# Performance work log

Hardware: AMD Instinct MI355X
Metric: run time of the kernel (lower is better)

## Reference

```python
import jax, jax.numpy as jnp
import numpy as np

N_NODES = 100000
N_EDGES = 1600000
NFEAT, NHID, NCLASS = 64, 128, 32


def _glorot(key, shape):
    fan_in, fan_out = shape[0], shape[1]
    lim = np.sqrt(6.0 / (fan_in + fan_out))
    return jax.random.uniform(key, shape, jnp.float32, -lim, lim)


def setup_inputs() -> dict:
    key = jax.random.key(0)
    ks = jax.random.split(key, 12)
    x = jax.random.normal(ks[0], (N_NODES, NFEAT), jnp.float32)
    edge_idx = jax.random.randint(ks[1], (2, N_EDGES), 0, N_NODES, jnp.int64)
    edge_weight = jax.random.uniform(ks[2], (N_EDGES,), jnp.float32)
    return {
        "x": x,
        "edge_idx": edge_idx,
        "edge_weight": edge_weight,
        # SAGEConv 1: out = mean_agg(x) @ Wl1 + b1 + x @ Wr1
        "Wl1": _glorot(ks[3], (NFEAT, NHID)),
        "Wr1": _glorot(ks[4], (NFEAT, NHID)),
        "b1": jnp.zeros((NHID,), jnp.float32),
        # SAGEConv 2
        "Wl2": _glorot(ks[5], (NHID, NHID)),
        "Wr2": _glorot(ks[6], (NHID, NHID)),
        "b2": jnp.zeros((NHID,), jnp.float32),
        # fc head: Linear(nhid, nclass) -> Linear(nclass, 1)
        "Wfc1": _glorot(ks[7], (NHID, NCLASS)),
        "bfc1": jnp.zeros((NCLASS,), jnp.float32),
        "Wfc2": _glorot(ks[8], (NCLASS, 1)),
        "bfc2": jnp.zeros((1,), jnp.float32),
    }


def _sage_conv(x, src, dst, Wl, Wr, b, n_nodes):
    # mean aggregation of source features at destination nodes
    msg_sum = jax.ops.segment_sum(x[src], dst, num_segments=n_nodes)  # [N, d]
    deg = jax.ops.segment_sum(jnp.ones((src.shape[0], 1), x.dtype), dst,
                              num_segments=n_nodes)                    # [N, 1]
    mean = msg_sum / jnp.maximum(deg, 1.0)
    return mean @ Wl + b + x @ Wr


def reference(x, edge_idx, edge_weight, Wl1, Wr1, b1, Wl2, Wr2, b2,
              Wfc1, bfc1, Wfc2, bfc2):
    n_nodes = x.shape[0]
    src, dst = edge_idx[0], edge_idx[1]
    # dropout is identity in eval mode (training=False)
    h = _sage_conv(x, src, dst, Wl1, Wr1, b1, n_nodes)   # [N, nhid]
    h = _sage_conv(h, src, dst, Wl2, Wr2, b2, n_nodes)   # [N, nhid]
    h = h @ Wfc1 + bfc1                                   # [N, nclass]
    out = h @ Wfc2 + bfc2                                 # [N, 1]
    return out
```

## Files before the change

### kernel.cpp

```cpp
#include <hip/hip_runtime.h>

#define S_SHIFT 9
#define S_NODES 512
#define CAP     10240
#define CHUNK   4096
#define NREP    4
#define DGRID   256

__global__ __launch_bounds__(1024) void fold_dots_kernel(
    const float* __restrict__ x,
    const float* __restrict__ Wl1, const float* __restrict__ Wr1, const float* __restrict__ b1,
    const float* __restrict__ Wl2, const float* __restrict__ Wr2, const float* __restrict__ b2,
    const float* __restrict__ Wfc1, const float* __restrict__ bfc1,
    const float* __restrict__ Wfc2, const float* __restrict__ bfc2,
    float* __restrict__ ga, float2* __restrict__ gbc, float* __restrict__ c01,
    int* __restrict__ cursor, int N)
{
    __shared__ float wv[192];
    __shared__ float uu[128], vl2[128], vr2[128], w2[32];
    int t = threadIdx.x;
    int l = t & 63;
    int w = t >> 6;

    if (blockIdx.x == 0 && t < 256) cursor[t] = 0;
    if (t < 32) w2[t] = Wfc2[t];
    __syncthreads();
    for (int j = 0; j < 8; ++j) {
        int i = w + 16 * j;
        float p = (l < 32) ? Wfc1[i * 32 + l] * w2[l] : 0.f;
        for (int m = 16; m; m >>= 1) p += __shfl_xor(p, m);
        if (l == 0) uu[i] = p;
    }
    __syncthreads();
    for (int j = 0; j < 8; ++j) {
        int i = w + 16 * j;
        float ua = uu[l], ub = uu[64 + l];
        float pa = Wl2[i * 128 + l] * ua + Wl2[i * 128 + 64 + l] * ub;
        float pb = Wr2[i * 128 + l] * ua + Wr2[i * 128 + 64 + l] * ub;
        for (int m = 32; m; m >>= 1) { pa += __shfl_xor(pa, m); pb += __shfl_xor(pb, m); }
        if (l == 0) { vl2[i] = pa; vr2[i] = pb; }
    }
    __syncthreads();
    for (int j = 0; j < 4; ++j) {
        int i = w + 16 * j;
        float l1a = Wl1[i * 128 + l], l1b = Wl1[i * 128 + 64 + l];
        float r1a = Wr1[i * 128 + l], r1b = Wr1[i * 128 + 64 + l];
        float La = vl2[l], Lb = vl2[64 + l], Ra = vr2[l], Rb = vr2[64 + l];
        float pc = l1a * La + l1b * Lb;
        float pb = l1a * Ra + l1b * Rb + r1a * La + r1b * Lb;
        float pa = r1a * Ra + r1b * Rb;
        for (int m = 32; m; m >>= 1) {
            pa += __shfl_xor(pa, m); pb += __shfl_xor(pb, m); pc += __shfl_xor(pc, m);
        }
        if (l == 0) { wv[i] = pa; wv[64 + i] = pb; wv[128 + i] = pc; }
    }
    if (blockIdx.x == 0 && w == 15) {
        float p0 = b1[l] * vr2[l] + b1[64 + l] * vr2[64 + l]
                 + b2[l] * uu[l] + b2[64 + l] * uu[64 + l];
        if (l < 32) p0 += bfc1[l] * w2[l];
        float p1 = b1[l] * vl2[l] + b1[64 + l] * vl2[64 + l];
        for (int m = 32; m; m >>= 1) { p0 += __shfl_xor(p0, m); p1 += __shfl_xor(p1, m); }
        if (l == 0) { c01[0] = p0 + bfc2[0]; c01[1] = p1; }
    }
    __syncthreads();

    int fp = l & 15, sub = l >> 4;
    float4 wa4 = ((const float4*)wv)[fp];
    float4 wb4 = ((const float4*)wv)[16 + fp];
    float4 wc4 = ((const float4*)wv)[32 + fp];
    const float4* x4 = (const float4*)x;
    int Q = (N + 3) >> 2;
    for (int qd = blockIdx.x * 16 + w; qd < Q; qd += DGRID * 16) {
        int node = qd * 4 + sub;
        float a = 0.f, b = 0.f, c = 0.f;
        if (node < N) {
            float4 v = x4[(size_t)node * 16 + fp];
            a = v.x * wa4.x + v.y * wa4.y + v.z * wa4.z + v.w * wa4.w;
            b = v.x * wb4.x + v.y * wb4.y + v.z * wb4.z + v.w * wb4.w;
            c = v.x * wc4.x + v.y * wc4.y + v.z * wc4.z + v.w * wc4.w;
        }
        for (int m = 8; m; m >>= 1) {
            a += __shfl_xor(a, m); b += __shfl_xor(b, m); c += __shfl_xor(c, m);
        }
        if (fp == 0 && node < N) { ga[node] = a; gbc[node] = make_float2(b, c); }
    }
}

__global__ __launch_bounds__(256) void scatter_kernel(
    const int* __restrict__ src, const int* __restrict__ dst, int E, int B,
    int* __restrict__ cursor, unsigned* __restrict__ bucket)
{
    __shared__ int hist[256], lbase[256], lcur[256];
    int t = threadIdx.x;
    int e0 = blockIdx.x * CHUNK;
    int cnt = E - e0; if (cnt > CHUNK) cnt = CHUNK;
    hist[t] = 0;
    __syncthreads();
    for (int i = t; i < cnt; i += 256)
        atomicAdd(&hist[dst[e0 + i] >> S_SHIFT], 1);
    __syncthreads();
    if (t < B && hist[t] > 0) lbase[t] = atomicAdd(&cursor[t], hist[t]);
    lcur[t] = 0;
    __syncthreads();
    for (int i = t; i < cnt; i += 256) {
        int d = dst[e0 + i], s = src[e0 + i];
        int b = d >> S_SHIFT;
        int off = atomicAdd(&lcur[b], 1);
        bucket[(size_t)b * CAP + (unsigned)(lbase[b] + off)] =
            ((unsigned)s << S_SHIFT) | (unsigned)(d & (S_NODES - 1));
    }
}

__global__ __launch_bounds__(1024) void aggA_kernel(
    const unsigned* __restrict__ bucket, const int* __restrict__ cursor,
    const float2* __restrict__ gbc, const float* __restrict__ ga,
    const float* __restrict__ c01,
    float* __restrict__ q, float* __restrict__ t1, float* __restrict__ inv, int N)
{
    __shared__ float aB[NREP][S_NODES], aC[NREP][S_NODES];
    __shared__ int cnt[NREP][S_NODES];
    int t = threadIdx.x, b = blockIdx.x;
    int r = (t >> 6) & (NREP - 1);
    float* aBf = (float*)aB; float* aCf = (float*)aC; int* cnf = (int*)cnt;
    for (int i = t; i < NREP * S_NODES; i += 1024) { aBf[i] = 0.f; aCf[i] = 0.f; cnf[i] = 0; }
    __syncthreads();
    int n = cursor[b];
    const unsigned* bp = bucket + (size_t)b * CAP;
    for (int i = t; i < n; i += 1024) {
        unsigned uu = bp[i];
        float2 g = gbc[uu >> S_SHIFT];
        int dl = uu & (S_NODES - 1);
        atomicAdd(&aB[r][dl], g.x);
        atomicAdd(&aC[r][dl], g.y);
        atomicAdd(&cnt[r][dl], 1);
    }
    __syncthreads();
    if (t < S_NODES) {
        int node = (b << S_SHIFT) + t;
        if (node < N) {
            float sb = aB[0][t] + aB[1][t] + aB[2][t] + aB[3][t];
            float sc = aC[0][t] + aC[1][t] + aC[2][t] + aC[3][t];
            int d = cnt[0][t] + cnt[1][t] + cnt[2][t] + cnt[3][t];
            float iv = 1.0f / ((d > 0) ? (float)d : 1.0f);
            inv[node] = iv;
            q[node]   = iv * sc;
            t1[node]  = ga[node] + iv * sb + c01[0] + (d > 0 ? c01[1] : 0.f);
        }
    }
}

__global__ __launch_bounds__(1024) void aggB_kernel(
    const unsigned* __restrict__ bucket, const int* __restrict__ cursor,
    const float* __restrict__ q, const float* __restrict__ t1,
    const float* __restrict__ inv, float* __restrict__ out, int N)
{
    __shared__ float a2[NREP][S_NODES];
    int t = threadIdx.x, b = blockIdx.x;
    int r = (t >> 6) & (NREP - 1);
    float* a2f = (float*)a2;
    for (int i = t; i < NREP * S_NODES; i += 1024) a2f[i] = 0.f;
    __syncthreads();
    int n = cursor[b];
    const unsigned* bp = bucket + (size_t)b * CAP;
    for (int i = t; i < n; i += 1024) {
        unsigned uu = bp[i];
        atomicAdd(&a2[r][uu & (S_NODES - 1)], q[uu >> S_SHIFT]);
    }
    __syncthreads();
    if (t < S_NODES) {
        int node = (b << S_SHIFT) + t;
        if (node < N)
            out[node] = t1[node] + inv[node] * (a2[0][t] + a2[1][t] + a2[2][t] + a2[3][t]);
    }
}

extern "C" void kernel_launch(void* const* d_in, const int* in_sizes, int n_in,
                              void* d_out, int out_size, void* d_ws, size_t ws_size,
                              hipStream_t stream) {
    const float* x    = (const float*)d_in[0];
    const int*   eidx = (const int*)d_in[1];
    const float* Wl1  = (const float*)d_in[3];
    const float* Wr1  = (const float*)d_in[4];
    const float* b1   = (const float*)d_in[5];
    const float* Wl2  = (const float*)d_in[6];
    const float* Wr2  = (const float*)d_in[7];
    const float* b2   = (const float*)d_in[8];
    const float* Wfc1 = (const float*)d_in[9];
    const float* bfc1 = (const float*)d_in[10];
    const float* Wfc2 = (const float*)d_in[11];
    const float* bfc2 = (const float*)d_in[12];

    const int N = in_sizes[0] / 64;
    const int E = in_sizes[2];
    const int* src = eidx;
    const int* dst = eidx + E;
    const int B = (N + S_NODES - 1) / S_NODES;
    const int nscat = (E + CHUNK - 1) / CHUNK;

    char* ws = (char*)d_ws;
    int*      cursor = (int*)(ws);
    float*    c01    = (float*)(ws + 1024);
    float*    ga     = (float*)(ws + 2048);
    float*    q      = (float*)(ws + 2048 + (size_t)N * 4);
    float*    t1     = (float*)(ws + 2048 + (size_t)N * 8);
    float*    inv    = (float*)(ws + 2048 + (size_t)N * 12);
    float2*   gbc    = (float2*)(ws + 2048 + (size_t)N * 16);
    unsigned* bucket = (unsigned*)(ws + 2048 + (size_t)N * 24);

    fold_dots_kernel<<<DGRID, 1024, 0, stream>>>(
        x, Wl1, Wr1, b1, Wl2, Wr2, b2, Wfc1, bfc1, Wfc2, bfc2,
        ga, gbc, c01, cursor, N);

    scatter_kernel<<<nscat, 256, 0, stream>>>(src, dst, E, B, cursor, bucket);

    aggA_kernel<<<B, 1024, 0, stream>>>(bucket, cursor, gbc, ga, c01, q, t1, inv, N);
    aggB_kernel<<<B, 1024, 0, stream>>>(bucket, cursor, q, t1, inv, (float*)d_out, N);
}
```

Before: 174.5 us.

## Fuse edge scatter and node dot-products into one kernel with smaller buckets

Merges the weight-folding/dot-product kernel and the edge bucketing scatter into one launch, with disjoint block ranges doing each job, so the two independent phases overlap and one launch is saved. The cursor reset becomes a memset because the fused kernel cannot zero it before the scatter blocks use it. Buckets shrink from 512 to 256 nodes (400 buckets, smaller capacity) and the aggregation kernels move to 512 threads, giving more blocks for load balance. The cost is an extra memset launch and a higher risk of bucket overflow with the smaller capacity under skewed degree distributions.

```diff
diff --git a/kernel.cpp b/kernel.cpp
--- a/kernel.cpp
+++ b/kernel.cpp
@@ -1,117 +1,117 @@
 #include <hip/hip_runtime.h>
 
-#define S_SHIFT 9
-#define S_NODES 512
-#define CAP     10240
-#define CHUNK   4096
+#define S_SHIFT 8
+#define S_NODES 256
+#define NBKT    400
+#define CAP     5120
+#define CHUNK   8192
 #define NREP    4
-#define DGRID   256
-
-__global__ __launch_bounds__(1024) void fold_dots_kernel(
+#define FTH     512
+#define NDOTS   160
+
+__global__ __launch_bounds__(FTH) void fused_kernel(
     const float* __restrict__ x,
+    const int* __restrict__ src, const int* __restrict__ dst,
+    int E, int N, int B, int nscat,
+    int* __restrict__ cursor, unsigned* __restrict__ bucket,
     const float* __restrict__ Wl1, const float* __restrict__ Wr1, const float* __restrict__ b1,
     const float* __restrict__ Wl2, const float* __restrict__ Wr2, const float* __restrict__ b2,
     const float* __restrict__ Wfc1, const float* __restrict__ bfc1,
     const float* __restrict__ Wfc2, const float* __restrict__ bfc2,
-    float* __restrict__ ga, float2* __restrict__ gbc, float* __restrict__ c01,
-    int* __restrict__ cursor, int N)
+    float* __restrict__ ga, float2* __restrict__ gbc, float* __restrict__ c01)
 {
-    __shared__ float wv[192];
-    __shared__ float uu[128], vl2[128], vr2[128], w2[32];
+    __shared__ int hist[NBKT], lbase[NBKT], lcur[NBKT];
+    __shared__ float wv[192], uu[128], vl2[128], vr2[128], w2[32];
     int t = threadIdx.x;
     int l = t & 63;
     int w = t >> 6;
 
-    if (blockIdx.x == 0 && t < 256) cursor[t] = 0;
-    if (t < 32) w2[t] = Wfc2[t];
-    __syncthreads();
-    for (int j = 0; j < 8; ++j) {
-        int i = w + 16 * j;
-        float p = (l < 32) ? Wfc1[i * 32 + l] * w2[l] : 0.f;
-        for (int m = 16; m; m >>= 1) p += __shfl_xor(p, m);
-        if (l == 0) uu[i] = p;
-    }
-    __syncthreads();
-    for (int j = 0; j < 8; ++j) {
-        int i = w + 16 * j;
-        float ua = uu[l], ub = uu[64 + l];
-        float pa = Wl2[i * 128 + l] * ua + Wl2[i * 128 + 64 + l] * ub;
-        float pb = Wr2[i * 128 + l] * ua + Wr2[i * 128 + 64 + l] * ub;
-        for (int m = 32; m; m >>= 1) { pa += __shfl_xor(pa, m); pb += __shfl_xor(pb, m); }
-        if (l == 0) { vl2[i] = pa; vr2[i] = pb; }
-    }
-    __syncthreads();
-    for (int j = 0; j < 4; ++j) {
-        int i = w + 16 * j;
-        float l1a = Wl1[i * 128 + l], l1b = Wl1[i * 128 + 64 + l];
-        float r1a = Wr1[i * 128 + l], r1b = Wr1[i * 128 + 64 + l];
-        float La = vl2[l], Lb = vl2[64 + l], Ra = vr2[l], Rb = vr2[64 + l];
-        float pc = l1a * La + l1b * Lb;
-        float pb = l1a * Ra + l1b * Rb + r1a * La + r1b * Lb;
-        float pa = r1a * Ra + r1b * Rb;
-        for (int m = 32; m; m >>= 1) {
-            pa += __shfl_xor(pa, m); pb += __shfl_xor(pb, m); pc += __shfl_xor(pc, m);
-        }
-        if (l == 0) { wv[i] = pa; wv[64 + i] = pb; wv[128 + i] = pc; }
-    }
-    if (blockIdx.x == 0 && w == 15) {
-        float p0 = b1[l] * vr2[l] + b1[64 + l] * vr2[64 + l]
-                 + b2[l] * uu[l] + b2[64 + l] * uu[64 + l];
-        if (l < 32) p0 += bfc1[l] * w2[l];
-        float p1 = b1[l] * vl2[l] + b1[64 + l] * vl2[64 + l];
-        for (int m = 32; m; m >>= 1) { p0 += __shfl_xor(p0, m); p1 += __shfl_xor(p1, m); }
-        if (l == 0) { c01[0] = p0 + bfc2[0]; c01[1] = p1; }
-    }
-    __syncthreads();
-
-    int fp = l & 15, sub = l >> 4;
-    float4 wa4 = ((const float4*)wv)[fp];
-    float4 wb4 = ((const float4*)wv)[16 + fp];
-    float4 wc4 = ((const float4*)wv)[32 + fp];
-    const float4* x4 = (const float4*)x;
-    int Q = (N + 3) >> 2;
-    for (int qd = blockIdx.x * 16 + w; qd < Q; qd += DGRID * 16) {
-        int node = qd * 4 + sub;
-        float a = 0.f, b = 0.f, c = 0.f;
-        if (node < N) {
-            float4 v = x4[(size_t)node * 16 + fp];
-            a = v.x * wa4.x + v.y * wa4.y + v.z * wa4.z + v.w * wa4.w;
-            b = v.x * wb4.x + v.y * wb4.y + v.z * wb4.z + v.w * wb4.w;
-            c = v.x * wc4.x + v.y * wc4.y + v.z * wc4.z + v.w * wc4.w;
-        }
-        for (int m = 8; m; m >>= 1) {
-            a += __shfl_xor(a, m); b += __shfl_xor(b, m); c += __shfl_xor(c, m);
-        }
-        if (fp == 0 && node < N) { ga[node] = a; gbc[node] = make_float2(b, c); }
-    }
-}
-
-__global__ __launch_bounds__(256) void scatter_kernel(
-    const int* __restrict__ src, const int* __restrict__ dst, int E, int B,
-    int* __restrict__ cursor, unsigned* __restrict__ bucket)
-{
-    __shared__ int hist[256], lbase[256], lcur[256];
-    int t = threadIdx.x;
-    int e0 = blockIdx.x * CHUNK;
-    int cnt = E - e0; if (cnt > CHUNK) cnt = CHUNK;
-    hist[t] = 0;
-    __syncthreads();
-    for (int i = t; i < cnt; i += 256)
-        atomicAdd(&hist[dst[e0 + i] >> S_SHIFT], 1);
-    __syncthreads();
-    if (t < B && hist[t] > 0) lbase[t] = atomicAdd(&cursor[t], hist[t]);
-    lcur[t] = 0;
-    __syncthreads();
-    for (int i = t; i < cnt; i += 256) {
-        int d = dst[e0 + i], s = src[e0 + i];
-        int b = d >> S_SHIFT;
-        int off = atomicAdd(&lcur[b], 1);
-        bucket[(size_t)b * CAP + (unsigned)(lbase[b] + off)] =
-            ((unsigned)s << S_SHIFT) | (unsigned)(d & (S_NODES - 1));
-    }
-}
-
-__global__ __launch_bounds__(1024) void aggA_kernel(
+    if ((int)blockIdx.x < nscat) {
+        int e0 = blockIdx.x * CHUNK;
+        int cnt = E - e0; if (cnt > CHUNK) cnt = CHUNK;
+        for (int i = t; i < B; i += FTH) hist[i] = 0;
+        __syncthreads();
+        for (int i = t; i < cnt; i += FTH)
+            atomicAdd(&hist[dst[e0 + i] >> S_SHIFT], 1);
+        __syncthreads();
+        for (int i = t; i < B; i += FTH) {
+            lcur[i] = 0;
+            if (hist[i] > 0) lbase[i] = atomicAdd(&cursor[i], hist[i]);
+        }
+        __syncthreads();
+        for (int i = t; i < cnt; i += FTH) {
+            int d = dst[e0 + i], s = src[e0 + i];
+            int bb = d >> S_SHIFT;
+            int off = atomicAdd(&lcur[bb], 1);
+            bucket[(size_t)bb * CAP + (unsigned)(lbase[bb] + off)] =
+                ((unsigned)s << S_SHIFT) | (unsigned)(d & (S_NODES - 1));
+        }
+    } else {
+        if (t < 32) w2[t] = Wfc2[t];
+        __syncthreads();
+        for (int j = 0; j < 16; ++j) {
+            int i = w + 8 * j;
+            float p = (l < 32) ? Wfc1[i * 32 + l] * w2[l] : 0.f;
+            for (int m = 16; m; m >>= 1) p += __shfl_xor(p, m);
+            if (l == 0) uu[i] = p;
+        }
+        __syncthreads();
+        for (int j = 0; j < 16; ++j) {
+            int i = w + 8 * j;
+            float ua = uu[l], ub = uu[64 + l];
+            float pa = Wl2[i * 128 + l] * ua + Wl2[i * 128 + 64 + l] * ub;
+            float pb = Wr2[i * 128 + l] * ua + Wr2[i * 128 + 64 + l] * ub;
+            for (int m = 32; m; m >>= 1) { pa += __shfl_xor(pa, m); pb += __shfl_xor(pb, m); }
+            if (l == 0) { vl2[i] = pa; vr2[i] = pb; }
+        }
+        __syncthreads();
+        for (int j = 0; j < 8; ++j) {
+            int i = w + 8 * j;
+            float l1a = Wl1[i * 128 + l], l1b = Wl1[i * 128 + 64 + l];
+            float r1a = Wr1[i * 128 + l], r1b = Wr1[i * 128 + 64 + l];
+            float La = vl2[l], Lb = vl2[64 + l], Ra = vr2[l], Rb = vr2[64 + l];
+            float pc = l1a * La + l1b * Lb;
+            float pb = l1a * Ra + l1b * Rb + r1a * La + r1b * Lb;
+            float pa = r1a * Ra + r1b * Rb;
+            for (int m = 32; m; m >>= 1) {
+                pa += __shfl_xor(pa, m); pb += __shfl_xor(pb, m); pc += __shfl_xor(pc, m);
+            }
+            if (l == 0) { wv[i] = pa; wv[64 + i] = pb; wv[128 + i] = pc; }
+        }
+        if ((int)blockIdx.x == nscat && w == 7) {
+            float p0 = b1[l] * vr2[l] + b1[64 + l] * vr2[64 + l]
+                     + b2[l] * uu[l] + b2[64 + l] * uu[64 + l];
+            if (l < 32) p0 += bfc1[l] * w2[l];
+            float p1 = b1[l] * vl2[l] + b1[64 + l] * vl2[64 + l];
+            for (int m = 32; m; m >>= 1) { p0 += __shfl_xor(p0, m); p1 += __shfl_xor(p1, m); }
+            if (l == 0) { c01[0] = p0 + bfc2[0]; c01[1] = p1; }
+        }
+        __syncthreads();
+
+        int fp = l & 15, sub = l >> 4;
+        float4 wa4 = ((const float4*)wv)[fp];
+        float4 wb4 = ((const float4*)wv)[16 + fp];
+        float4 wc4 = ((const float4*)wv)[32 + fp];
+        const float4* x4 = (const float4*)x;
+        int Q = (N + 3) >> 2;
+        for (int qd = ((int)blockIdx.x - nscat) * 8 + w; qd < Q; qd += NDOTS * 8) {
+            int node = qd * 4 + sub;
+            float a = 0.f, b = 0.f, c = 0.f;
+            if (node < N) {
+                float4 v = x4[(size_t)node * 16 + fp];
+                a = v.x * wa4.x + v.y * wa4.y + v.z * wa4.z + v.w * wa4.w;
+                b = v.x * wb4.x + v.y * wb4.y + v.z * wb4.z + v.w * wb4.w;
+                c = v.x * wc4.x + v.y * wc4.y + v.z * wc4.z + v.w * wc4.w;
+            }
+            for (int m = 8; m; m >>= 1) {
+                a += __shfl_xor(a, m); b += __shfl_xor(b, m); c += __shfl_xor(c, m);
+            }
+            if (fp == 0 && node < N) { ga[node] = a; gbc[node] = make_float2(b, c); }
+        }
+    }
+}
+
+__global__ __launch_bounds__(512) void aggA_kernel(
     const unsigned* __restrict__ bucket, const int* __restrict__ cursor,
     const float2* __restrict__ gbc, const float* __restrict__ ga,
     const float* __restrict__ c01,
@@ -122,11 +122,11 @@
     int t = threadIdx.x, b = blockIdx.x;
     int r = (t >> 6) & (NREP - 1);
     float* aBf = (float*)aB; float* aCf = (float*)aC; int* cnf = (int*)cnt;
-    for (int i = t; i < NREP * S_NODES; i += 1024) { aBf[i] = 0.f; aCf[i] = 0.f; cnf[i] = 0; }
+    for (int i = t; i < NREP * S_NODES; i += 512) { aBf[i] = 0.f; aCf[i] = 0.f; cnf[i] = 0; }
     __syncthreads();
     int n = cursor[b];
     const unsigned* bp = bucket + (size_t)b * CAP;
-    for (int i = t; i < n; i += 1024) {
+    for (int i = t; i < n; i += 512) {
         unsigned uu = bp[i];
         float2 g = gbc[uu >> S_SHIFT];
         int dl = uu & (S_NODES - 1);
@@ -149,7 +149,7 @@
     }
 }
 
-__global__ __launch_bounds__(1024) void aggB_kernel(
+__global__ __launch_bounds__(512) void aggB_kernel(
     const unsigned* __restrict__ bucket, const int* __restrict__ cursor,
     const float* __restrict__ q, const float* __restrict__ t1,
     const float* __restrict__ inv, float* __restrict__ out, int N)
@@ -158,11 +158,11 @@
     int t = threadIdx.x, b = blockIdx.x;
     int r = (t >> 6) & (NREP - 1);
     float* a2f = (float*)a2;
-    for (int i = t; i < NREP * S_NODES; i += 1024) a2f[i] = 0.f;
+    for (int i = t; i < NREP * S_NODES; i += 512) a2f[i] = 0.f;
     __syncthreads();
     int n = cursor[b];
     const unsigned* bp = bucket + (size_t)b * CAP;
-    for (int i = t; i < n; i += 1024) {
+    for (int i = t; i < n; i += 512) {
         unsigned uu = bp[i];
         atomicAdd(&a2[r][uu & (S_NODES - 1)], q[uu >> S_SHIFT]);
     }
@@ -199,20 +199,21 @@
 
     char* ws = (char*)d_ws;
     int*      cursor = (int*)(ws);
-    float*    c01    = (float*)(ws + 1024);
-    float*    ga     = (float*)(ws + 2048);
-    float*    q      = (float*)(ws + 2048 + (size_t)N * 4);
-    float*    t1     = (float*)(ws + 2048 + (size_t)N * 8);
-    float*    inv    = (float*)(ws + 2048 + (size_t)N * 12);
-    float2*   gbc    = (float2*)(ws + 2048 + (size_t)N * 16);
-    unsigned* bucket = (unsigned*)(ws + 2048 + (size_t)N * 24);
-
-    fold_dots_kernel<<<DGRID, 1024, 0, stream>>>(
-        x, Wl1, Wr1, b1, Wl2, Wr2, b2, Wfc1, bfc1, Wfc2, bfc2,
-        ga, gbc, c01, cursor, N);
-
-    scatter_kernel<<<nscat, 256, 0, stream>>>(src, dst, E, B, cursor, bucket);
-
-    aggA_kernel<<<B, 1024, 0, stream>>>(bucket, cursor, gbc, ga, c01, q, t1, inv, N);
-    aggB_kernel<<<B, 1024, 0, stream>>>(bucket, cursor, q, t1, inv, (float*)d_out, N);
-}
+    float*    c01    = (float*)(ws + 2048);
+    float*    ga     = (float*)(ws + 4096);
+    float*    q      = (float*)(ws + 4096 + (size_t)N * 4);
+    float*    t1     = (float*)(ws + 4096 + (size_t)N * 8);
+    float*    inv    = (float*)(ws + 4096 + (size_t)N * 12);
+    float2*   gbc    = (float2*)(ws + 4096 + (size_t)N * 16);
+    unsigned* bucket = (unsigned*)(ws + 4096 + (size_t)N * 24);
+
+    hipMemsetAsync(cursor, 0, 2048, stream);
+
+    fused_kernel<<<nscat + NDOTS, FTH, 0, stream>>>(
+        x, src, dst, E, N, B, nscat, cursor, bucket,
+        Wl1, Wr1, b1, Wl2, Wr2, b2, Wfc1, bfc1, Wfc2, bfc2,
+        ga, gbc, c01);
+
+    aggA_kernel<<<B, 512, 0, stream>>>(bucket, cursor, gbc, ga, c01, q, t1, inv, N);
+    aggB_kernel<<<B, 512, 0, stream>>>(bucket, cursor, q, t1, inv, (float*)d_out, N);
+}
```

New measurement: 171.1 us. -2.0%, faster.
